# Optimization experiments

Measured on AMD Instinct MI355X. Metric: run time of the kernel, lower is better.

## Reference

```python
import jax, jax.numpy as jnp
import numpy as np

B, Q, C, H, D, E, I = 8, 256, 192, 20, 64, 1500, 5120
HID = H * D  # 1280
EPS = 1e-5
SCALE = D ** -0.5


def _linear(x, w, b):
    return jnp.einsum('bsh,oh->bso', x, w) + b


def _layernorm(x, w, b):
    xf = x.astype(jnp.float32)
    mu = jnp.mean(xf, axis=-1, keepdims=True)
    var = jnp.mean(jnp.square(xf - mu), axis=-1, keepdims=True)
    return ((xf - mu) * jax.lax.rsqrt(var + EPS) * w + b).astype(x.dtype)


def _heads(x):  # [B,S,HID] -> [B,H,S,D]
    return x.reshape(B, -1, H, D).transpose(0, 2, 1, 3)


def setup_inputs() -> dict:
    key = jax.random.key(0)
    ks = jax.random.split(key, 24)
    s = 0.02
    inp = {
        'hidden_states': jax.random.normal(ks[0], (B, Q, HID), jnp.float32),
        'mask': jnp.zeros((B, 1, Q, Q + C), jnp.float32),
        'past_key': jax.random.normal(ks[1], (B, H, C, D), jnp.float32),
        'past_value': jax.random.normal(ks[2], (B, H, C, D), jnp.float32),
        'cross_key': jax.random.normal(ks[3], (B, H, E, D), jnp.float32),
        'cross_value': jax.random.normal(ks[4], (B, H, E, D), jnp.float32),
        'q_w': jax.random.normal(ks[5], (HID, HID), jnp.float32) * s,
        'q_b': jnp.zeros((HID,), jnp.float32),
        'k_w': jax.random.normal(ks[6], (HID, HID), jnp.float32) * s,
        'k_b': jnp.zeros((HID,), jnp.float32),
        'v_w': jax.random.normal(ks[7], (HID, HID), jnp.float32) * s,
        'v_b': jnp.zeros((HID,), jnp.float32),
        'o_w': jax.random.normal(ks[8], (HID, HID), jnp.float32) * s,
        'o_b': jnp.zeros((HID,), jnp.float32),
        'cq_w': jax.random.normal(ks[9], (HID, HID), jnp.float32) * s,
        'cq_b': jnp.zeros((HID,), jnp.float32),
        'co_w': jax.random.normal(ks[10], (HID, HID), jnp.float32) * s,
        'co_b': jnp.zeros((HID,), jnp.float32),
        'up_w': jax.random.normal(ks[11], (I, HID), jnp.float32) * s,
        'up_b': jnp.zeros((I,), jnp.float32),
        'down_w': jax.random.normal(ks[12], (HID, I), jnp.float32) * s,
        'down_b': jnp.zeros((HID,), jnp.float32),
        'ln1_w': jnp.ones((HID,), jnp.float32),
        'ln1_b': jnp.zeros((HID,), jnp.float32),
        'ln2_w': jnp.ones((HID,), jnp.float32),
        'ln2_b': jnp.zeros((HID,), jnp.float32),
        'ln3_w': jnp.ones((HID,), jnp.float32),
        'ln3_b': jnp.zeros((HID,), jnp.float32),
    }
    return inp


def reference(hidden_states, mask, past_key, past_value, cross_key, cross_value,
              q_w, q_b, k_w, k_b, v_w, v_b, o_w, o_b,
              cq_w, cq_b, co_w, co_b, up_w, up_b, down_w, down_b,
              ln1_w, ln1_b, ln2_w, ln2_b, ln3_w, ln3_b):
    # ---- self-attention block ----
    residual = hidden_states
    x = _layernorm(hidden_states, ln1_w, ln1_b)
    q = _heads(_linear(x, q_w, q_b) * SCALE)          # [B,H,Q,D]
    k_new = _heads(_linear(x, k_w, k_b))              # [B,H,Q,D]
    v_new = _heads(_linear(x, v_w, v_b))
    k = jnp.concatenate([past_key, k_new], axis=2)    # [B,H,C+Q,D]
    v = jnp.concatenate([past_value, v_new], axis=2)
    scores = jnp.einsum('bhqd,bhkd->bhqk', q, k) + mask
    attn = jnp.einsum('bhqk,bhkd->bhqd', jax.nn.softmax(scores, axis=-1), v)
    attn = attn.transpose(0, 2, 1, 3).reshape(B, Q, HID)
    attn_out = _linear(attn, o_w, o_b)
    present_key = k[:, :, Q:, :]
    present_value = v[:, :, Q:, :]
    h = residual + attn_out
    # ---- cross-attention block ----
    residual = h
    x = _layernorm(h, ln2_w, ln2_b)
    cq = _heads(_linear(x, cq_w, cq_b) * SCALE)       # [B,H,Q,D]
    cscores = jnp.einsum('bhqd,bhkd->bhqk', cq, cross_key)
    cattn = jnp.einsum('bhqk,bhkd->bhqd', jax.nn.softmax(cscores, axis=-1), cross_value)
    cattn = cattn.transpose(0, 2, 1, 3).reshape(B, Q, HID)
    h = residual + _linear(cattn, co_w, co_b)
    # ---- MLP block ----
    residual = h
    x = _layernorm(h, ln3_w, ln3_b)
    up = _linear(x, up_w, up_b)
    mlp_out = _linear(jax.nn.gelu(up, approximate=False), down_w, down_b)
    h = residual + mlp_out
    return (h, present_key, present_value)
```

## Files before the change

kernel.cpp:

```cpp
#include <hip/hip_runtime.h>
#include <math.h>

#define Bc   8
#define Qn   256
#define Cn   192
#define Hn   20
#define Dn   64
#define En   1500
#define In   5120
#define HIDn 1280
#define BQ   2048
#define KSELF 448
#define EPAD 1536
#define S1   (BQ*HIDn)
#define WSZ  (HIDn*HIDn)
#define BH   (Bc*Hn)

typedef __attribute__((ext_vector_type(8))) short bf16x8;
typedef __attribute__((ext_vector_type(4))) float f32x4;

__device__ __forceinline__ short f2bf(float f) {
  union { float f; unsigned u; } x; x.f = f;
  unsigned r = x.u + 0x7fffu + ((x.u >> 16) & 1u);
  return (short)(r >> 16);
}
__device__ __forceinline__ float bf2f(short s) {
  union { unsigned u; float f; } x; x.u = ((unsigned)(unsigned short)s) << 16;
  return x.f;
}
__device__ __forceinline__ void gload16(const short* g, short* l) {
  __builtin_amdgcn_global_load_lds(
      (const __attribute__((address_space(1))) void*)g,
      (__attribute__((address_space(3))) void*)l, 16, 0, 0);
}
__device__ __forceinline__ bf16x8 cvt8(const float* p) {
  const float4 a = *reinterpret_cast<const float4*>(p);
  const float4 b = *reinterpret_cast<const float4*>(p + 4);
  bf16x8 t;
  t[0] = f2bf(a.x); t[1] = f2bf(a.y); t[2] = f2bf(a.z); t[3] = f2bf(a.w);
  t[4] = f2bf(b.x); t[5] = f2bf(b.y); t[6] = f2bf(b.z); t[7] = f2bf(b.w);
  return t;
}

__global__ __launch_bounds__(256) void convert_all(
    const float* q, const float* k, const float* v, const float* o,
    const float* cq, const float* co, const float* up, const float* dn,
    short* wq, short* wk, short* wv, short* wo,
    short* wcq, short* wco, short* wup, short* wdn)
{
  const float* src; short* dst; int n;
  switch (blockIdx.y) {
    case 0: src = q;  dst = wq;  n = WSZ; break;
    case 1: src = k;  dst = wk;  n = WSZ; break;
    case 2: src = v;  dst = wv;  n = WSZ; break;
    case 3: src = o;  dst = wo;  n = WSZ; break;
    case 4: src = cq; dst = wcq; n = WSZ; break;
    case 5: src = co; dst = wco; n = WSZ; break;
    case 6: src = up; dst = wup; n = HIDn * In; break;
    default: src = dn; dst = wdn; n = HIDn * In; break;
  }
  const int i = (blockIdx.x * 256 + threadIdx.x) * 8;
  if (i >= n) return;
  *reinterpret_cast<bf16x8*>(dst + i) = cvt8(src + i);
}

__global__ __launch_bounds__(256) void prep_cross(
    const float* __restrict__ K, const float* __restrict__ V,
    short* __restrict__ Kc, short* __restrict__ Vc)
{
  const size_t idx = (size_t)blockIdx.x * 256 + threadIdx.x;
  const int d8 = (int)(idx & 7) * 8;
  const size_t t = idx >> 3;
  const int key = (int)(t % EPAD);
  const int bh  = (int)(t / EPAD);
  bf16x8 kv = (bf16x8)0, vv = (bf16x8)0;
  if (key < En) {
    const size_t off = ((size_t)bh * En + key) * 64 + d8;
    kv = cvt8(K + off);
    vv = cvt8(V + off);
  }
  const size_t dst = ((size_t)bh * EPAD + key) * 64 + d8;
  *reinterpret_cast<bf16x8*>(Kc + dst) = kv;
  *reinterpret_cast<bf16x8*>(Vc + dst) = vv;
}

__global__ __launch_bounds__(256) void prep_self(
    const float* __restrict__ Kp, const float* __restrict__ Vp,
    const short* __restrict__ kn, const short* __restrict__ vn,
    short* __restrict__ Kc, short* __restrict__ Vc)
{
  const size_t idx = (size_t)blockIdx.x * 256 + threadIdx.x;
  const int d8 = (int)(idx & 7) * 8;
  const size_t t = idx >> 3;
  const int key = (int)(t % KSELF);
  const int bh  = (int)(t / KSELF);
  bf16x8 kv, vv;
  if (key < Cn) {
    const size_t off = ((size_t)bh * Cn + key) * 64 + d8;
    kv = cvt8(Kp + off);
    vv = cvt8(Vp + off);
  } else {
    const int b = bh / Hn, h = bh % Hn;
    const size_t off = ((size_t)(b * Qn + (key - Cn))) * HIDn + h * 64 + d8;
    kv = *reinterpret_cast<const bf16x8*>(kn + off);
    vv = *reinterpret_cast<const bf16x8*>(vn + off);
  }
  const size_t dst = ((size_t)bh * KSELF + key) * 64 + d8;
  *reinterpret_cast<bf16x8*>(Kc + dst) = kv;
  *reinterpret_cast<bf16x8*>(Vc + dst) = vv;
}

__global__ __launch_bounds__(256) void layernorm_k(
    const float* __restrict__ in, const float* __restrict__ w,
    const float* __restrict__ b, short* __restrict__ out)
{
  const int row = blockIdx.x;
  const float* x = in + (size_t)row * HIDn;
  float v[5], s = 0.f, s2 = 0.f;
#pragma unroll
  for (int i = 0; i < 5; ++i) {
    float t = x[threadIdx.x + 256 * i];
    v[i] = t; s += t; s2 += t * t;
  }
#pragma unroll
  for (int off = 1; off < 64; off <<= 1) {
    s  += __shfl_xor(s,  off, 64);
    s2 += __shfl_xor(s2, off, 64);
  }
  __shared__ float red[8];
  const int wave = threadIdx.x >> 6, lane = threadIdx.x & 63;
  if (lane == 0) { red[wave] = s; red[wave + 4] = s2; }
  __syncthreads();
  s  = red[0] + red[1] + red[2] + red[3];
  s2 = red[4] + red[5] + red[6] + red[7];
  const float mu  = s / HIDn;
  const float var = s2 / HIDn - mu * mu;
  const float rs  = rsqrtf(var + 1e-5f);
#pragma unroll
  for (int i = 0; i < 5; ++i) {
    const int c = threadIdx.x + 256 * i;
    out[(size_t)row * HIDn + c] = f2bf((v[i] - mu) * rs * w[c] + b[c]);
  }
}

template<int BM, int BN, int MODE>
__global__ __launch_bounds__(256) void gemm_bk64(
    const short* __restrict__ A, const short* __restrict__ W,
    const float* __restrict__ bias, const float* __restrict__ resid,
    void* __restrict__ out0, void* __restrict__ out1, void* __restrict__ out2,
    const float* __restrict__ b1, const float* __restrict__ b2,
    int N, int K, int LDK, float scale)
{
  constexpr int FM = BM / 32, FN = BN / 32;
  __shared__ __align__(16) short Alds[BM * 64];
  __shared__ __align__(16) short Blds[BN * 64];
  const int tid = threadIdx.x, lane = tid & 63, wave = tid >> 6;
  const int wr = wave >> 1, wc = wave & 1;
  const int m0 = blockIdx.x * BM, n0 = blockIdx.y * BN;
  const int bz = blockIdx.z;
  const int lr = lane & 15;
  const int kc = (lane >> 4) * 8;
  const size_t koff = (size_t)bz * K;

  f32x4 acc[FM][FN];
#pragma unroll
  for (int mi = 0; mi < FM; ++mi)
#pragma unroll
    for (int ni = 0; ni < FN; ++ni)
      acc[mi][ni] = (f32x4){0.f, 0.f, 0.f, 0.f};

  const int nk = K >> 6;
  for (int kt = 0; kt < nk; ++kt) {
    const int k0 = kt << 6;
#pragma unroll
    for (int j = 0; j < BM / 32; ++j) {
      const int i = wave + 4 * j;
      const int rb = i >> 1, kk = i & 1;
      gload16(A + (size_t)(m0 + rb * 16 + lr) * LDK + koff + k0 + kk * 32 + kc,
              &Alds[i * 512]);
    }
#pragma unroll
    for (int j = 0; j < BN / 32; ++j) {
      const int i = wave + 4 * j;
      const int rb = i >> 1, kk = i & 1;
      gload16(W + (size_t)(n0 + rb * 16 + lr) * LDK + koff + k0 + kk * 32 + kc,
              &Blds[i * 512]);
    }
    __syncthreads();
    bf16x8 af[2][FM], bfv[2][FN];
#pragma unroll
    for (int kk = 0; kk < 2; ++kk) {
#pragma unroll
      for (int mi = 0; mi < FM; ++mi)
        af[kk][mi] = *reinterpret_cast<const bf16x8*>(
            &Alds[((wr * FM + mi) * 2 + kk) * 512 + lane * 8]);
#pragma unroll
      for (int ni = 0; ni < FN; ++ni)
        bfv[kk][ni] = *reinterpret_cast<const bf16x8*>(
            &Blds[((wc * FN + ni) * 2 + kk) * 512 + lane * 8]);
    }
#pragma unroll
    for (int kk = 0; kk < 2; ++kk)
#pragma unroll
      for (int mi = 0; mi < FM; ++mi)
#pragma unroll
        for (int ni = 0; ni < FN; ++ni)
          acc[mi][ni] = __builtin_amdgcn_mfma_f32_16x16x32_bf16(
              af[kk][mi], bfv[kk][ni], acc[mi][ni], 0, 0, 0);
    __syncthreads();
  }

  const int cn = lane & 15;
  const int rb = (lane >> 4) * 4;
#pragma unroll
  for (int mi = 0; mi < FM; ++mi)
#pragma unroll
    for (int ni = 0; ni < FN; ++ni)
#pragma unroll
      for (int j = 0; j < 4; ++j) {
        const int row = m0 + wr * (BM / 2) + mi * 16 + rb + j;
        const int col = n0 + wc * (BN / 2) + ni * 16 + cn;
        const float a = acc[mi][ni][j];
        if (MODE == 0) {
          ((float*)out0)[(size_t)row * N + col] =
              a + bias[col] + resid[(size_t)row * N + col];
        } else if (MODE == 1) {
          ((short*)out0)[(size_t)row * N + col] = f2bf((a + bias[col]) * scale);
        } else if (MODE == 2) {
          float t = a + bias[col];
          t = 0.5f * t * (1.f + erff(t * 0.70710678118654752f));
          ((short*)out0)[(size_t)row * N + col] = f2bf(t);
        } else if (MODE == 3) {
          const int rg  = n0 / 1280;
          const int cl  = col - rg * 1280;
          short* op     = rg == 0 ? (short*)out0 : rg == 1 ? (short*)out1 : (short*)out2;
          const float* bp = rg == 0 ? bias : rg == 1 ? b1 : b2;
          const float sc  = rg == 0 ? 0.125f : 1.f;
          op[(size_t)row * 1280 + cl] = f2bf((a + bp[cl]) * sc);
        } else {
          float* op = bz == 0 ? (float*)out0 : (float*)out1;
          op[(size_t)row * N + col] = a;
        }
      }
}

__global__ __launch_bounds__(256) void reduce_down(
    const float* __restrict__ p0, const float* __restrict__ p1,
    const float* __restrict__ resid, const float* __restrict__ bias,
    float* __restrict__ out)
{
  const size_t i = ((size_t)blockIdx.x * 256 + threadIdx.x) * 4;
  if (i >= (size_t)S1) return;
  const int col = (int)(i % HIDn);
  const float4 a = *reinterpret_cast<const float4*>(p0 + i);
  const float4 b = *reinterpret_cast<const float4*>(p1 + i);
  const float4 r = *reinterpret_cast<const float4*>(resid + i);
  const float4 bi = *reinterpret_cast<const float4*>(bias + col);
  float4 o;
  o.x = a.x + b.x + r.x + bi.x;
  o.y = a.y + b.y + r.y + bi.y;
  o.z = a.z + b.z + r.z + bi.z;
  o.w = a.w + b.w + r.w + bi.w;
  *reinterpret_cast<float4*>(out + i) = o;
}

template<bool HASMASK>
__global__ __launch_bounds__(256) void attn_mfma(
    const short* __restrict__ Qb, const short* __restrict__ Kc,
    const short* __restrict__ Vc, const float* __restrict__ mask,
    short* __restrict__ Ob, int PADK, int KT)
{
  const int orig = blockIdx.x;
  const int idx  = (orig & 7) * 80 + (orig >> 3);
  const int qt = idx & 3;
  const int h  = (idx >> 2) % Hn;
  const int b  = idx / (4 * Hn);
  const int bh = b * Hn + h;
  const int tid = threadIdx.x, lane = tid & 63, wave = tid >> 6;
  const int q0 = qt * 64;
  const int cn = lane & 15;
  const int hg = lane >> 4;
  const int rb = hg * 4;

  __shared__ __align__(16) short k_s[64][72];
  __shared__ __align__(16) short vt_s[64][72];
  __shared__ __align__(16) short p_s[4][16][72];

  bf16x8 aq[2];
  {
    const short* qrow = Qb + (size_t)(b * Qn + q0 + wave * 16 + cn) * HIDn + h * 64;
    aq[0] = *reinterpret_cast<const bf16x8*>(qrow + hg * 8);
    aq[1] = *reinterpret_cast<const bf16x8*>(qrow + 32 + hg * 8);
  }

  float mrun[4] = {-1e30f, -1e30f, -1e30f, -1e30f};
  float lrun[4] = {0.f, 0.f, 0.f, 0.f};
  f32x4 oacc[4];
#pragma unroll
  for (int t = 0; t < 4; ++t) oacc[t] = (f32x4){0.f, 0.f, 0.f, 0.f};

  const int nchunk = PADK >> 6;
  for (int ci = 0; ci < nchunk; ++ci) {
    const int c0 = ci * 64;
    const short* kbase = Kc + ((size_t)bh * PADK + c0) * 64;
    const short* vbase = Vc + ((size_t)bh * PADK + c0) * 64;
#pragma unroll
    for (int r = 0; r < 2; ++r) {
      const int i = tid + r * 256;
      const int key = i >> 3, d8 = (i & 7) * 8;
      const bf16x8 kv = *reinterpret_cast<const bf16x8*>(kbase + key * 64 + d8);
      const bf16x8 vv = *reinterpret_cast<const bf16x8*>(vbase + key * 64 + d8);
      *reinterpret_cast<bf16x8*>(&k_s[key][d8]) = kv;
      const int g = key >> 3, o = key & 7, f = i & 7;
      const int col = ((g ^ f) << 3) | o;
#pragma unroll
      for (int j = 0; j < 8; ++j) vt_s[d8 + j][col] = vv[j];
    }
    __syncthreads();

    f32x4 sacc[4];
#pragma unroll
    for (int t = 0; t < 4; ++t) sacc[t] = (f32x4){0.f, 0.f, 0.f, 0.f};
#pragma unroll
    for (int t = 0; t < 4; ++t)
#pragma unroll
      for (int kk = 0; kk < 2; ++kk) {
        const bf16x8 bk = *reinterpret_cast<const bf16x8*>(&k_s[t * 16 + cn][kk * 32 + hg * 8]);
        sacc[t] = __builtin_amdgcn_mfma_f32_16x16x32_bf16(aq[kk], bk, sacc[t], 0, 0, 0);
      }

    float sc[4][4];
#pragma unroll
    for (int t = 0; t < 4; ++t) {
      const int key = c0 + t * 16 + cn;
      const bool valid = key < KT;
#pragma unroll
      for (int j = 0; j < 4; ++j) {
        float v = sacc[t][j];
        if (HASMASK && valid)
          v += mask[((size_t)(b * Qn) + q0 + wave * 16 + rb + j) * KT + key];
        sc[t][j] = valid ? v : -1e30f;
      }
    }

#pragma unroll
    for (int j = 0; j < 4; ++j) {
      float mx = fmaxf(fmaxf(sc[0][j], sc[1][j]), fmaxf(sc[2][j], sc[3][j]));
#pragma unroll
      for (int off = 1; off < 16; off <<= 1) mx = fmaxf(mx, __shfl_xor(mx, off, 64));
      if (mx > mrun[j] + 8.f) {
        const float alpha = __expf(mrun[j] - mx);
        lrun[j] *= alpha;
#pragma unroll
        for (int t = 0; t < 4; ++t) oacc[t][j] *= alpha;
        mrun[j] = mx;
      }
      float ps = 0.f;
#pragma unroll
      for (int t = 0; t < 4; ++t) {
        const float p = __expf(sc[t][j] - mrun[j]);
        sc[t][j] = p; ps += p;
      }
#pragma unroll
      for (int off = 1; off < 16; off <<= 1) ps += __shfl_xor(ps, off, 64);
      lrun[j] += ps;
    }

#pragma unroll
    for (int t = 0; t < 4; ++t)
#pragma unroll
      for (int j = 0; j < 4; ++j)
        p_s[wave][rb + j][t * 16 + cn] = f2bf(sc[t][j]);

    const bf16x8 ap0 = *reinterpret_cast<const bf16x8*>(&p_s[wave][cn][hg * 8]);
    const bf16x8 ap1 = *reinterpret_cast<const bf16x8*>(&p_s[wave][cn][32 + hg * 8]);
#pragma unroll
    for (int t = 0; t < 4; ++t) {
      const int d  = t * 16 + cn;
      const int fd = (d >> 3) & 7;
      const bf16x8 bv0 = *reinterpret_cast<const bf16x8*>(&vt_s[d][((hg)     ^ fd) << 3]);
      const bf16x8 bv1 = *reinterpret_cast<const bf16x8*>(&vt_s[d][((4 + hg) ^ fd) << 3]);
      oacc[t] = __builtin_amdgcn_mfma_f32_16x16x32_bf16(ap0, bv0, oacc[t], 0, 0, 0);
      oacc[t] = __builtin_amdgcn_mfma_f32_16x16x32_bf16(ap1, bv1, oacc[t], 0, 0, 0);
    }
    __syncthreads();
  }

#pragma unroll
  for (int t = 0; t < 4; ++t)
#pragma unroll
    for (int j = 0; j < 4; ++j)
      Ob[(size_t)(b * Qn + q0 + wave * 16 + rb + j) * HIDn + h * 64 + t * 16 + cn] =
          f2bf(oacc[t][j] / lrun[j]);
}

__global__ __launch_bounds__(256) void copy_present(
    const short* __restrict__ kn, const short* __restrict__ vn,
    float* __restrict__ outk, float* __restrict__ outv)
{
  const int idx = blockIdx.x * 256 + threadIdx.x;
  if (idx >= Bc * Hn * Cn * 8) return;
  const int d8 = (idx & 7) * 8;
  int t = idx >> 3;
  const int c = t % Cn; t /= Cn;
  const int h = t % Hn;
  const int b = t / Hn;
  const size_t src = (size_t)(b * Qn + (Qn - Cn) + c) * HIDn + h * 64 + d8;
  const size_t dst = (((size_t)b * Hn + h) * Cn + c) * 64 + d8;
  const bf16x8 kv = *reinterpret_cast<const bf16x8*>(kn + src);
  const bf16x8 vv = *reinterpret_cast<const bf16x8*>(vn + src);
#pragma unroll
  for (int j = 0; j < 8; ++j) {
    outk[dst + j] = bf2f(kv[j]);
    outv[dst + j] = bf2f(vv[j]);
  }
}

extern "C" void kernel_launch(void* const* d_in, const int* in_sizes, int n_in,
                              void* d_out, int out_size, void* d_ws, size_t ws_size,
                              hipStream_t stream)
{
  const float* hidden  = (const float*)d_in[0];
  const float* mask    = (const float*)d_in[1];
  const float* past_k  = (const float*)d_in[2];
  const float* past_v  = (const float*)d_in[3];
  const float* cross_k = (const float*)d_in[4];
  const float* cross_v = (const float*)d_in[5];
  const float* q_w  = (const float*)d_in[6];  const float* q_b  = (const float*)d_in[7];
  const float* k_w  = (const float*)d_in[8];  const float* k_b  = (const float*)d_in[9];
  const float* v_w  = (const float*)d_in[10]; const float* v_b  = (const float*)d_in[11];
  const float* o_w  = (const float*)d_in[12]; const float* o_b  = (const float*)d_in[13];
  const float* cq_w = (const float*)d_in[14]; const float* cq_b = (const float*)d_in[15];
  const float* co_w = (const float*)d_in[16]; const float* co_b = (const float*)d_in[17];
  const float* up_w = (const float*)d_in[18]; const float* up_b = (const float*)d_in[19];
  const float* dn_w = (const float*)d_in[20]; const float* dn_b = (const float*)d_in[21];
  const float* ln1w = (const float*)d_in[22]; const float* ln1b = (const float*)d_in[23];
  const float* ln2w = (const float*)d_in[24]; const float* ln2b = (const float*)d_in[25];
  const float* ln3w = (const float*)d_in[26]; const float* ln3b = (const float*)d_in[27];

  short* wq  = (short*)d_ws;
  short* wk  = wq  + (size_t)WSZ;
  short* wv  = wk  + (size_t)WSZ;
  short* wo  = wv  + (size_t)WSZ;
  short* wcq = wo  + (size_t)WSZ;
  short* wco = wcq + (size_t)WSZ;
  short* wup = wco + (size_t)WSZ;
  short* wdn = wup + (size_t)HIDn * In;
  short* xb  = wdn + (size_t)HIDn * In;
  short* qb  = xb  + (size_t)S1;
  short* kb  = qb  + (size_t)S1;
  short* vb  = kb  + (size_t)S1;
  short* ab  = vb  + (size_t)S1;
  short* U   = ab  + (size_t)S1;
  short* ksb = U;
  short* vsb = U + (size_t)BH * KSELF * 64;
  short* upa = U;
  short* kcc = U + (size_t)BQ * In;
  short* vcc = kcc + (size_t)BH * EPAD * 64;
  float* h1  = (float*)(vcc + (size_t)BH * EPAD * 64);
  float* p0  = (float*)qb;
  float* p1  = (float*)vb;

  float* out_h  = (float*)d_out;
  float* out_pk = out_h + (size_t)S1;
  float* out_pv = out_pk + (size_t)(Bc * Hn * Cn * Dn);
  float* h2 = out_h;

  const dim3 blk(256);
  const dim3 gconv(3200, 8);
  const dim3 gqkv(16, 30);
  const dim3 gn64(16, 20);
  const dim3 gup(16, 40);
  const dim3 gdn(16, 20, 2);
  const dim3 gattn(640);

  convert_all<<<gconv, blk, 0, stream>>>(q_w, k_w, v_w, o_w, cq_w, co_w, up_w, dn_w,
                                         wq, wk, wv, wo, wcq, wco, wup, wdn);
  prep_cross<<<(BH * EPAD * 8) / 256, blk, 0, stream>>>(cross_k, cross_v, kcc, vcc);
  layernorm_k<<<BQ, blk, 0, stream>>>(hidden, ln1w, ln1b, xb);
  gemm_bk64<128, 128, 3><<<gqkv, blk, 0, stream>>>(xb, wq, q_b, nullptr,
      qb, kb, vb, k_b, v_b, 3840, HIDn, HIDn, 1.f);
  copy_present<<<(Bc * Hn * Cn * 8 + 255) / 256, blk, 0, stream>>>(kb, vb, out_pk, out_pv);
  prep_self<<<(BH * KSELF * 8) / 256, blk, 0, stream>>>(past_k, past_v, kb, vb, ksb, vsb);
  attn_mfma<true><<<gattn, blk, 0, stream>>>(qb, ksb, vsb, mask, ab, KSELF, KSELF);
  gemm_bk64<128, 64, 0><<<gn64, blk, 0, stream>>>(ab, wo, o_b, hidden,
      h1, nullptr, nullptr, nullptr, nullptr, HIDn, HIDn, HIDn, 1.f);
  layernorm_k<<<BQ, blk, 0, stream>>>(h1, ln2w, ln2b, xb);
  gemm_bk64<128, 64, 1><<<gn64, blk, 0, stream>>>(xb, wcq, cq_b, nullptr,
      qb, nullptr, nullptr, nullptr, nullptr, HIDn, HIDn, HIDn, 0.125f);
  attn_mfma<false><<<gattn, blk, 0, stream>>>(qb, kcc, vcc, nullptr, ab, EPAD, En);
  gemm_bk64<128, 64, 0><<<gn64, blk, 0, stream>>>(ab, wco, co_b, h1,
      h2, nullptr, nullptr, nullptr, nullptr, HIDn, HIDn, HIDn, 1.f);
  layernorm_k<<<BQ, blk, 0, stream>>>(h2, ln3w, ln3b, xb);
  gemm_bk64<128, 128, 2><<<gup, blk, 0, stream>>>(xb, wup, up_b, nullptr,
      upa, nullptr, nullptr, nullptr, nullptr, In, HIDn, HIDn, 1.f);
  gemm_bk64<128, 64, 4><<<gdn, blk, 0, stream>>>(upa, wdn, nullptr, nullptr,
      p0, p1, nullptr, nullptr, nullptr, HIDn, In / 2, In, 1.f);
  reduce_down<<<(S1 / 4 + 255) / 256, blk, 0, stream>>>(p0, p1, h2, dn_b, out_h);
}
```

Baseline: 539.7 us.

## Double-buffer GEMM LDS tiles and split-K the 1280x1280 projections

```diff
diff --git a/kernel.cpp b/kernel.cpp
--- a/kernel.cpp
+++ b/kernel.cpp
@@ -144,7 +144,7 @@
 }
 
 template<int BM, int BN, int MODE>
-__global__ __launch_bounds__(256) void gemm_bk64(
+__global__ __launch_bounds__(256) void gemm_db(
     const short* __restrict__ A, const short* __restrict__ W,
     const float* __restrict__ bias, const float* __restrict__ resid,
     void* __restrict__ out0, void* __restrict__ out1, void* __restrict__ out2,
@@ -152,8 +152,8 @@
     int N, int K, int LDK, float scale)
 {
   constexpr int FM = BM / 32, FN = BN / 32;
-  __shared__ __align__(16) short Alds[BM * 64];
-  __shared__ __align__(16) short Blds[BN * 64];
+  __shared__ __align__(16) short Alds[2][BM * 64];
+  __shared__ __align__(16) short Blds[2][BN * 64];
   const int tid = threadIdx.x, lane = tid & 63, wave = tid >> 6;
   const int wr = wave >> 1, wc = wave & 1;
   const int m0 = blockIdx.x * BM, n0 = blockIdx.y * BN;
@@ -169,35 +169,44 @@
     for (int ni = 0; ni < FN; ++ni)
       acc[mi][ni] = (f32x4){0.f, 0.f, 0.f, 0.f};
 
-  const int nk = K >> 6;
-  for (int kt = 0; kt < nk; ++kt) {
+  auto STAGE = [&](int kt, int buf) {
     const int k0 = kt << 6;
 #pragma unroll
     for (int j = 0; j < BM / 32; ++j) {
       const int i = wave + 4 * j;
-      const int rb = i >> 1, kk = i & 1;
-      gload16(A + (size_t)(m0 + rb * 16 + lr) * LDK + koff + k0 + kk * 32 + kc,
-              &Alds[i * 512]);
+      const int rr = i >> 1, kk = i & 1;
+      gload16(A + (size_t)(m0 + rr * 16 + lr) * LDK + koff + k0 + kk * 32 + kc,
+              &Alds[buf][i * 512]);
     }
 #pragma unroll
     for (int j = 0; j < BN / 32; ++j) {
       const int i = wave + 4 * j;
-      const int rb = i >> 1, kk = i & 1;
-      gload16(W + (size_t)(n0 + rb * 16 + lr) * LDK + koff + k0 + kk * 32 + kc,
-              &Blds[i * 512]);
-    }
-    __syncthreads();
+      const int rr = i >> 1, kk = i & 1;
+      gload16(W + (size_t)(n0 + rr * 16 + lr) * LDK + koff + k0 + kk * 32 + kc,
+              &Blds[buf][i * 512]);
+    }
+  };
+
+  const int nk = K >> 6;
+  STAGE(0, 0);
+  asm volatile("s_waitcnt vmcnt(0)" ::: "memory");
+  __builtin_amdgcn_s_barrier();
+  __builtin_amdgcn_sched_barrier(0);
+
+  int cur = 0;
+  for (int kt = 0; kt < nk; ++kt) {
+    if (kt + 1 < nk) STAGE(kt + 1, cur ^ 1);
     bf16x8 af[2][FM], bfv[2][FN];
 #pragma unroll
     for (int kk = 0; kk < 2; ++kk) {
 #pragma unroll
       for (int mi = 0; mi < FM; ++mi)
         af[kk][mi] = *reinterpret_cast<const bf16x8*>(
-            &Alds[((wr * FM + mi) * 2 + kk) * 512 + lane * 8]);
+            &Alds[cur][((wr * FM + mi) * 2 + kk) * 512 + lane * 8]);
 #pragma unroll
       for (int ni = 0; ni < FN; ++ni)
         bfv[kk][ni] = *reinterpret_cast<const bf16x8*>(
-            &Blds[((wc * FN + ni) * 2 + kk) * 512 + lane * 8]);
+            &Blds[cur][((wc * FN + ni) * 2 + kk) * 512 + lane * 8]);
     }
 #pragma unroll
     for (int kk = 0; kk < 2; ++kk)
@@ -207,7 +216,11 @@
         for (int ni = 0; ni < FN; ++ni)
           acc[mi][ni] = __builtin_amdgcn_mfma_f32_16x16x32_bf16(
               af[kk][mi], bfv[kk][ni], acc[mi][ni], 0, 0, 0);
-    __syncthreads();
+    __builtin_amdgcn_sched_barrier(0);
+    asm volatile("s_waitcnt vmcnt(0)" ::: "memory");
+    __builtin_amdgcn_s_barrier();
+    __builtin_amdgcn_sched_barrier(0);
+    cur ^= 1;
   }
 
   const int cn = lane & 15;
@@ -244,24 +257,31 @@
       }
 }
 
-__global__ __launch_bounds__(256) void reduce_down(
+template<int RM>
+__global__ __launch_bounds__(256) void reduce_k(
     const float* __restrict__ p0, const float* __restrict__ p1,
     const float* __restrict__ resid, const float* __restrict__ bias,
-    float* __restrict__ out)
+    float* __restrict__ outf, short* __restrict__ outb, float scale)
 {
   const size_t i = ((size_t)blockIdx.x * 256 + threadIdx.x) * 4;
   if (i >= (size_t)S1) return;
   const int col = (int)(i % HIDn);
-  const float4 a = *reinterpret_cast<const float4*>(p0 + i);
-  const float4 b = *reinterpret_cast<const float4*>(p1 + i);
-  const float4 r = *reinterpret_cast<const float4*>(resid + i);
+  const float4 a  = *reinterpret_cast<const float4*>(p0 + i);
+  const float4 b  = *reinterpret_cast<const float4*>(p1 + i);
   const float4 bi = *reinterpret_cast<const float4*>(bias + col);
-  float4 o;
-  o.x = a.x + b.x + r.x + bi.x;
-  o.y = a.y + b.y + r.y + bi.y;
-  o.z = a.z + b.z + r.z + bi.z;
-  o.w = a.w + b.w + r.w + bi.w;
-  *reinterpret_cast<float4*>(out + i) = o;
+  if (RM == 0) {
+    const float4 r = *reinterpret_cast<const float4*>(resid + i);
+    float4 o;
+    o.x = a.x + b.x + bi.x + r.x;
+    o.y = a.y + b.y + bi.y + r.y;
+    o.z = a.z + b.z + bi.z + r.z;
+    o.w = a.w + b.w + bi.w + r.w;
+    *reinterpret_cast<float4*>(outf + i) = o;
+  } else {
+    *reinterpret_cast<short4*>(outb + i) = make_short4(
+        f2bf((a.x + b.x + bi.x) * scale), f2bf((a.y + b.y + bi.y) * scale),
+        f2bf((a.z + b.z + bi.z) * scale), f2bf((a.w + b.w + bi.w) * scale));
+  }
 }
 
 template<bool HASMASK>
@@ -455,11 +475,13 @@
   short* ksb = U;
   short* vsb = U + (size_t)BH * KSELF * 64;
   short* upa = U;
+  float* po0 = (float*)U;
+  float* po1 = po0 + (size_t)S1;
   short* kcc = U + (size_t)BQ * In;
   short* vcc = kcc + (size_t)BH * EPAD * 64;
   float* h1  = (float*)(vcc + (size_t)BH * EPAD * 64);
-  float* p0  = (float*)qb;
-  float* p1  = (float*)vb;
+  float* pd0 = (float*)qb;
+  float* pd1 = (float*)vb;
 
   float* out_h  = (float*)d_out;
   float* out_pk = out_h + (size_t)S1;
@@ -469,32 +491,35 @@
   const dim3 blk(256);
   const dim3 gconv(3200, 8);
   const dim3 gqkv(16, 30);
-  const dim3 gn64(16, 20);
+  const dim3 gsplit(16, 20, 2);
   const dim3 gup(16, 40);
-  const dim3 gdn(16, 20, 2);
   const dim3 gattn(640);
+  const dim3 gred((S1 / 4 + 255) / 256);
 
   convert_all<<<gconv, blk, 0, stream>>>(q_w, k_w, v_w, o_w, cq_w, co_w, up_w, dn_w,
                                          wq, wk, wv, wo, wcq, wco, wup, wdn);
   prep_cross<<<(BH * EPAD * 8) / 256, blk, 0, stream>>>(cross_k, cross_v, kcc, vcc);
   layernorm_k<<<BQ, blk, 0, stream>>>(hidden, ln1w, ln1b, xb);
-  gemm_bk64<128, 128, 3><<<gqkv, blk, 0, stream>>>(xb, wq, q_b, nullptr,
+  gemm_db<128, 128, 3><<<gqkv, blk, 0, stream>>>(xb, wq, q_b, nullptr,
       qb, kb, vb, k_b, v_b, 3840, HIDn, HIDn, 1.f);
   copy_present<<<(Bc * Hn * Cn * 8 + 255) / 256, blk, 0, stream>>>(kb, vb, out_pk, out_pv);
   prep_self<<<(BH * KSELF * 8) / 256, blk, 0, stream>>>(past_k, past_v, kb, vb, ksb, vsb);
   attn_mfma<true><<<gattn, blk, 0, stream>>>(qb, ksb, vsb, mask, ab, KSELF, KSELF);
-  gemm_bk64<128, 64, 0><<<gn64, blk, 0, stream>>>(ab, wo, o_b, hidden,
-      h1, nullptr, nullptr, nullptr, nullptr, HIDn, HIDn, HIDn, 1.f);
+  gemm_db<128, 64, 4><<<gsplit, blk, 0, stream>>>(ab, wo, nullptr, nullptr,
+      po0, po1, nullptr, nullptr, nullptr, HIDn, HIDn / 2, HIDn, 1.f);
+  reduce_k<0><<<gred, blk, 0, stream>>>(po0, po1, hidden, o_b, h1, nullptr, 1.f);
   layernorm_k<<<BQ, blk, 0, stream>>>(h1, ln2w, ln2b, xb);
-  gemm_bk64<128, 64, 1><<<gn64, blk, 0, stream>>>(xb, wcq, cq_b, nullptr,
-      qb, nullptr, nullptr, nullptr, nullptr, HIDn, HIDn, HIDn, 0.125f);
+  gemm_db<128, 64, 4><<<gsplit, blk, 0, stream>>>(xb, wcq, nullptr, nullptr,
+      po0, po1, nullptr, nullptr, nullptr, HIDn, HIDn / 2, HIDn, 1.f);
+  reduce_k<1><<<gred, blk, 0, stream>>>(po0, po1, nullptr, cq_b, nullptr, qb, 0.125f);
   attn_mfma<false><<<gattn, blk, 0, stream>>>(qb, kcc, vcc, nullptr, ab, EPAD, En);
-  gemm_bk64<128, 64, 0><<<gn64, blk, 0, stream>>>(ab, wco, co_b, h1,
-      h2, nullptr, nullptr, nullptr, nullptr, HIDn, HIDn, HIDn, 1.f);
+  gemm_db<128, 64, 4><<<gsplit, blk, 0, stream>>>(ab, wco, nullptr, nullptr,
+      po0, po1, nullptr, nullptr, nullptr, HIDn, HIDn / 2, HIDn, 1.f);
+  reduce_k<0><<<gred, blk, 0, stream>>>(po0, po1, h1, co_b, h2, nullptr, 1.f);
   layernorm_k<<<BQ, blk, 0, stream>>>(h2, ln3w, ln3b, xb);
-  gemm_bk64<128, 128, 2><<<gup, blk, 0, stream>>>(xb, wup, up_b, nullptr,
+  gemm_db<128, 128, 2><<<gup, blk, 0, stream>>>(xb, wup, up_b, nullptr,
       upa, nullptr, nullptr, nullptr, nullptr, In, HIDn, HIDn, 1.f);
-  gemm_bk64<128, 64, 4><<<gdn, blk, 0, stream>>>(upa, wdn, nullptr, nullptr,
-      p0, p1, nullptr, nullptr, nullptr, HIDn, In / 2, In, 1.f);
-  reduce_down<<<(S1 / 4 + 255) / 256, blk, 0, stream>>>(p0, p1, h2, dn_b, out_h);
-}
+  gemm_db<128, 64, 4><<<gsplit, blk, 0, stream>>>(upa, wdn, nullptr, nullptr,
+      pd0, pd1, nullptr, nullptr, nullptr, HIDn, In / 2, In, 1.f);
+  reduce_k<0><<<gred, blk, 0, stream>>>(pd0, pd1, h2, dn_b, out_h, nullptr, 1.f);
+}
```

Measured after the change: 541.7 us. Within noise of the previous version (+0.4%).
